# Kernel tuning notes

Measured on AMD Instinct MI355X. Metric: run time of the kernel, lower is better.

Reference implementation:

```python
import jax, jax.numpy as jnp
import numpy as np
from jax import lax

EPS = 1e-5
PH = PW = 2  # patch size

def _bn(x, g, b, m, v):
    # eval-mode BatchNorm2d on NCHW
    scale = (g / jnp.sqrt(v + EPS))[None, :, None, None]
    return (x - m[None, :, None, None]) * scale + b[None, :, None, None]

def _gn1(x, g, b):
    # GroupNorm(num_groups=1): normalize over (C,P,N) per sample
    mu = x.mean(axis=(1, 2, 3), keepdims=True)
    var = x.var(axis=(1, 2, 3), keepdims=True)
    return (x - mu) / jnp.sqrt(var + EPS) * g[None, :, None, None] + b[None, :, None, None]

def _conv1x1(x, w, b=None):
    y = jnp.einsum('oc,bcpn->bopn', w, x)
    if b is not None:
        y = y + b[None, :, None, None]
    return y

def _silu(x):
    return x * jax.nn.sigmoid(x)

def _lin_attn(x, qkv_w, qkv_b, out_w, out_b, D):
    # x: [B, D, P, N]
    qkv = _conv1x1(x, qkv_w, qkv_b)            # [B, 2D+1, P, N]
    q = qkv[:, :1]                              # [B, 1, P, N]
    k = qkv[:, 1:1 + D]                         # [B, D, P, N]
    v = qkv[:, 1 + D:]                          # [B, D, P, N]
    scores = jax.nn.softmax(q, axis=-1)         # softmax over patches N
    ctx = jnp.sum(k * scores, axis=-1, keepdims=True)  # [B, D, P, 1]
    out = jax.nn.relu(v) * ctx
    return _conv1x1(out, out_w, out_b)

def reference(x, dw_w, dw_bn_g, dw_bn_b, dw_bn_m, dw_bn_v, pw_w,
              gn1_g, gn1_b, qkv_w, qkv_b, out_w, out_b,
              gn2_g, gn2_b, ffn1_w, ffn1_b, ffn2_w, ffn2_b,
              gnf_g, gnf_b, proj_w, proj_bn_g, proj_bn_b, proj_bn_m, proj_bn_v):
    B, C, H, W = x.shape
    D = pw_w.shape[0]
    L = gn1_g.shape[0]
    # local representation: depthwise 3x3 conv + BN + SiLU, then 1x1 to attn dim
    y = lax.conv_general_dilated(x, dw_w, (1, 1), 'SAME',
                                 feature_group_count=C,
                                 dimension_numbers=('NCHW', 'OIHW', 'NCHW'))
    y = _silu(_bn(y, dw_bn_g, dw_bn_b, dw_bn_m, dw_bn_v))
    y = _conv1x1(y, pw_w)                       # [B, D, H, W]
    # unfold to [B, D, P, N] (non-overlapping patches, torch F.unfold ordering)
    nH, nW = H // PH, W // PW
    p = y.reshape(B, D, nH, PH, nW, PW).transpose(0, 1, 3, 5, 2, 4).reshape(B, D, PH * PW, nH * nW)
    # global representation: L pre-norm linear-attention + FFN blocks
    for i in range(L):
        p = p + _lin_attn(_gn1(p, gn1_g[i], gn1_b[i]), qkv_w[i], qkv_b[i], out_w[i], out_b[i], D)
        h = _gn1(p, gn2_g[i], gn2_b[i])
        h = _silu(_conv1x1(h, ffn1_w[i], ffn1_b[i]))
        h = _conv1x1(h, ffn2_w[i], ffn2_b[i])
        p = p + h
    p = _gn1(p, gnf_g, gnf_b)
    # fold back to [B, D, H, W]
    y = p.reshape(B, D, PH, PW, nH, nW).transpose(0, 1, 4, 2, 5, 3).reshape(B, D, H, W)
    # projection back to in_channels: 1x1 conv + BN (no act)
    y = _conv1x1(y, proj_w)
    y = _bn(y, proj_bn_g, proj_bn_b, proj_bn_m, proj_bn_v)
    return y

def setup_inputs() -> dict:
    key = jax.random.key(0)
    ks = iter(jax.random.split(key, 40))
    def rn(shape, s=0.05):
        return jax.random.normal(next(ks), shape, jnp.float32) * s
    B, C, H, W, D, F, L = 16, 256, 64, 64, 256, 512, 2
    return dict(
        x=jax.random.normal(next(ks), (B, C, H, W), jnp.float32),
        dw_w=rn((C, 1, 3, 3), 0.2),
        dw_bn_g=jnp.ones((C,), jnp.float32), dw_bn_b=jnp.zeros((C,), jnp.float32),
        dw_bn_m=rn((C,), 0.01), dw_bn_v=jnp.ones((C,), jnp.float32),
        pw_w=rn((D, C)),
        gn1_g=jnp.ones((L, D), jnp.float32), gn1_b=jnp.zeros((L, D), jnp.float32),
        qkv_w=rn((L, 2 * D + 1, D)), qkv_b=jnp.zeros((L, 2 * D + 1), jnp.float32),
        out_w=rn((L, D, D)), out_b=jnp.zeros((L, D), jnp.float32),
        gn2_g=jnp.ones((L, D), jnp.float32), gn2_b=jnp.zeros((L, D), jnp.float32),
        ffn1_w=rn((L, F, D)), ffn1_b=jnp.zeros((L, F), jnp.float32),
        ffn2_w=rn((L, D, F)), ffn2_b=jnp.zeros((L, D), jnp.float32),
        gnf_g=jnp.ones((D,), jnp.float32), gnf_b=jnp.zeros((D,), jnp.float32),
        proj_w=rn((C, D)),
        proj_bn_g=jnp.ones((C,), jnp.float32), proj_bn_b=jnp.zeros((C,), jnp.float32),
        proj_bn_m=rn((C,), 0.01), proj_bn_v=jnp.ones((C,), jnp.float32),
    )
```

## Files before the change

kernel.cpp:

```cpp
#include <hip/hip_runtime.h>
#include <hip/hip_bf16.h>
#include <stdint.h>


#define B_    16
#define C_    256
#define D_    256
#define NPIX  4096
#define NE_PB 1048576

typedef __attribute__((ext_vector_type(8))) short  short8;
typedef __attribute__((ext_vector_type(4))) short  short4v;
typedef __attribute__((ext_vector_type(4))) float  f32x4;
typedef __attribute__((ext_vector_type(2))) float  f32x2;

__device__ __forceinline__ float b2f(short s){
  return __uint_as_float(((unsigned)(unsigned short)s) << 16);
}
__device__ __forceinline__ short f2b(float f){
  __bf16 h = (__bf16)f;
  return *(short*)&h;
}
__device__ __forceinline__ float silu_f(float x){
  float e = __builtin_amdgcn_exp2f(-1.44269504f * x);
  return x * __builtin_amdgcn_rcpf(1.f + e);
}

__device__ __forceinline__ void gld16(const short* g, short* l){
  __builtin_amdgcn_global_load_lds(
      (const __attribute__((address_space(1))) void*)g,
      (__attribute__((address_space(3))) void*)l, 16, 0, 0);
}

__device__ __forceinline__ int pi2pix(int n){
  int p = n >> 10, idx = n & 1023;
  int h = ((idx >> 5) << 1) | (p >> 1);
  int w = ((idx & 31) << 1) | (p & 1);
  return h*64 + w;
}

__global__ void cvt6_k(const float* __restrict__ s0, const float* __restrict__ s1,
                       const float* __restrict__ s2, const float* __restrict__ s3,
                       const float* __restrict__ s4, const float* __restrict__ s5,
                       const float* __restrict__ g1, const float* __restrict__ g2,
                       const float* __restrict__ gf,
                       short* __restrict__ dst, float* __restrict__ stats){
  const int i = blockIdx.x*256 + threadIdx.x;
  if (blockIdx.x == 0 && threadIdx.x < 160) stats[threadIdx.x] = 0.f;
  if (i >= 1049088) return;
  float v;
  if      (i <  65536){ v = s0[i]; }
  else if (i < 328192){ int j = i -  65536;
                        v = s1[j] * g1[(j/131328)*256 + (j & 255)]; }
  else if (i < 459264){ v = s2[i - 328192]; }
  else if (i < 721408){ int j = i - 459264;
                        v = s3[j] * g2[(j >> 17)*256 + (j & 255)]; }
  else if (i < 983552){ v = s4[i - 721408]; }
  else               { int j = i - 983552;
                        v = s5[j] * gf[j & 255]; }
  dst[i] = f2b(v);
}

__global__ void fold_k(const float* __restrict__ qkvw, const float* __restrict__ f1w,
                       const float* __restrict__ pjw,
                       const float* __restrict__ g1, const float* __restrict__ b1,
                       const float* __restrict__ g2, const float* __restrict__ b2,
                       const float* __restrict__ gf, const float* __restrict__ bf,
                       float* __restrict__ uv){
  const int row = blockIdx.x;
  const int l = threadIdx.x;
  const float* W; const float* g; const float* bb;
  if (row < 1026){ int layer = row/513, o = row - layer*513;
    W = qkvw + (size_t)(layer*513 + o)*256; g = g1 + layer*256; bb = b1 + layer*256; }
  else if (row < 2050){ int r2 = row - 1026; int layer = r2 >> 9, o = r2 & 511;
    W = f1w + (size_t)(layer*512 + o)*256; g = g2 + layer*256; bb = b2 + layer*256; }
  else { int o = row - 2050; W = pjw + (size_t)o*256; g = gf; bb = bf; }
  float u = 0.f, v = 0.f;
#pragma unroll
  for (int k = 0; k < 4; ++k){
    const int c = l + k*64;
    const float w = W[c];
    u += w * g[c]; v += w * bb[c];
  }
#pragma unroll
  for (int o = 32; o > 0; o >>= 1){ u += __shfl_down(u, o); v += __shfl_down(v, o); }
  if (l == 0){ uv[row*2] = u; uv[row*2+1] = v; }
}

__global__ __launch_bounds__(256)
void dwconv_k(const float* __restrict__ X, const float* __restrict__ W,
              const float* __restrict__ G, const float* __restrict__ Bb,
              const float* __restrict__ Mn, const float* __restrict__ Vr,
              short* __restrict__ O){
  const int c = blockIdx.x, b = blockIdx.y;
  const int t = threadIdx.x;
  __shared__ float xs[66][68];
  if (t < 132){ int r = (t >= 66) ? 65 : 0; int cc = (t >= 66) ? t-66 : t; xs[r][cc] = 0.f; }
  if (t < 128){ int r = 1 + (t & 63); int cc = (t >> 6) ? 65 : 0; xs[r][cc] = 0.f; }
  const float* xp = X + ((size_t)(b*C_ + c)) * NPIX;
#pragma unroll
  for (int it = 0; it < 4; ++it){
    const int idx = it*256 + t;
    const int row = idx >> 4, cq = idx & 15;
    f32x4 v = *(const f32x4*)&xp[row*64 + cq*4];
    xs[row+1][cq*4+1] = v.x; xs[row+1][cq*4+2] = v.y;
    xs[row+1][cq*4+3] = v.z; xs[row+1][cq*4+4] = v.w;
  }
  float wgt[9];
#pragma unroll
  for (int j = 0; j < 9; ++j) wgt[j] = W[c*9 + j];
  const float scale = G[c] * rsqrtf(Vr[c] + 1e-5f);
  const float mu = Mn[c], bb = Bb[c];
  __syncthreads();
  const int tr = t >> 4, tc = t & 15;
  float win[6][6];
#pragma unroll
  for (int dr = 0; dr < 6; ++dr){
    f32x4 a = *(const f32x4*)&xs[tr*4+dr][tc*4];
    f32x2 bq = *(const f32x2*)&xs[tr*4+dr][tc*4+4];
    win[dr][0] = a.x; win[dr][1] = a.y; win[dr][2] = a.z; win[dr][3] = a.w;
    win[dr][4] = bq.x; win[dr][5] = bq.y;
  }
  short* op = O + ((size_t)(b*C_ + c)) * NPIX;
#pragma unroll
  for (int jr = 0; jr < 4; ++jr){
    short4v o;
#pragma unroll
    for (int jc = 0; jc < 4; ++jc){
      float s = 0.f;
#pragma unroll
      for (int dh = 0; dh < 3; ++dh)
#pragma unroll
        for (int dw = 0; dw < 3; ++dw)
          s += win[jr+dh][jc+dw] * wgt[dh*3+dw];
      float y = (s - mu) * scale + bb;
      o[jc] = f2b(silu_f(y));
    }
    *(short4v*)&op[(tr*4+jr)*64 + tc*4] = o;
  }
}

__global__ void transpose_k(const short* __restrict__ I, short* __restrict__ O){
  const int s0 = blockIdx.x*64, c0 = blockIdx.y*64, b = blockIdx.z;
  const int t = threadIdx.x;
  __shared__ short tile[64][68];
  const int hi = t >> 4, lo = t & 15;
#pragma unroll
  for (int cy = 0; cy < 4; ++cy){
    const int cl = cy*16 + hi;
    short4v v = *(const short4v*)&I[((size_t)(b*C_ + c0 + cl))*NPIX + s0 + lo*4];
    tile[lo*4+0][cl] = v.x; tile[lo*4+1][cl] = v.y;
    tile[lo*4+2][cl] = v.z; tile[lo*4+3][cl] = v.w;
  }
  __syncthreads();
#pragma unroll
  for (int py = 0; py < 4; ++py){
    const int pl = py*16 + hi;
    short4v v = *(const short4v*)&tile[pl][lo*4];
    *(short4v*)&O[((size_t)(b*NPIX + s0 + pl))*C_ + c0 + lo*4] = v;
  }
}

template<int EPI, int K, int FOLD, int GATHER>
__global__ __launch_bounds__(256, 3)
void gemm_k(const short* __restrict__ Wt, const short* __restrict__ X,
            const int M,
            const float* __restrict__ bias,
            short* __restrict__ P,
            short* __restrict__ Obf,
            float* __restrict__ Of32,
            const float* __restrict__ bng, const float* __restrict__ bnb,
            const float* __restrict__ bnm, const float* __restrict__ bnv,
            float* __restrict__ st,
            const float* __restrict__ uv, const float* __restrict__ stIn)
{
  constexpr int S = K / 64;
  const int nt = blockIdx.x;
  const int ct = blockIdx.y;
  const int b  = blockIdx.z;
  const int tid = threadIdx.x;
  const int ln = tid & 63, wv = tid >> 6;
  const int wx = wv & 1;
  const int wy = wv >> 1;
  const int lr = ln & 15, lq = ln >> 4;
  const int rl = ln >> 3, sp = ln & 7;
  const int sw = sp ^ rl;

  __shared__ __align__(16) char smem[33824];
  short* As = (short*)smem;
  short* Xs = (short*)(smem + 16384);
  float* CT = (float*)smem;
  float* red = (float*)(smem + 33792);

  const short* Wp = Wt + (size_t)(ct*128)*K;
  const short* Xp = X + ((size_t)b*NPIX + (size_t)nt*128) * K;

  const short* gw[4]; const short* gx[4]; short* lw[4]; short* lx[4];
#pragma unroll
  for (int j = 0; j < 4; ++j){
    const int row = 32*wv + 8*j + rl;
    gw[j] = Wp + (size_t)row*K + sw*8;
    if constexpr (GATHER)
      gx[j] = X + ((size_t)b*NPIX + pi2pix(nt*128 + row))*K + sw*8;
    else
      gx[j] = Xp + (size_t)row*K + sw*8;
    lw[j] = As + (4*wv + j)*512;
    lx[j] = Xs + (4*wv + j)*512;
  }

  f32x4 acc[4][4];
#pragma unroll
  for (int r = 0; r < 4; ++r)
#pragma unroll
    for (int c = 0; c < 4; ++c) acc[r][c] = (f32x4){0.f,0.f,0.f,0.f};

  for (int stp = 0; stp < S; ++stp){
    if (stp) __syncthreads();
#pragma unroll
    for (int j = 0; j < 4; ++j) gld16(gw[j] + stp*64, lw[j]);
#pragma unroll
    for (int j = 0; j < 4; ++j) gld16(gx[j] + stp*64, lx[j]);
    __syncthreads();
#pragma unroll
    for (int kk = 0; kk < 2; ++kk){
      const int seg = ((kk*4 + lq) ^ (lr & 7)) * 16;
      short8 aw[4], bx[4];
#pragma unroll
      for (int r = 0; r < 4; ++r)
        aw[r] = *(const short8*)((const char*)As + (wx*64 + r*16 + lr)*128 + seg);
#pragma unroll
      for (int c = 0; c < 4; ++c)
        bx[c] = *(const short8*)((const char*)Xs + (wy*64 + c*16 + lr)*128 + seg);
#pragma unroll
      for (int r = 0; r < 4; ++r)
#pragma unroll
        for (int c = 0; c < 4; ++c)
          acc[r][c] = __builtin_amdgcn_mfma_f32_16x16x32_bf16(aw[r], bx[c], acc[r][c], 0, 0, 0);
    }
  }

  const int ch8 = (tid & 15) * 8;
  float s_mul = 1.f;
  f32x4 be0 = (f32x4){0.f,0.f,0.f,0.f}, be1 = be0;
  if constexpr (EPI == 1 || EPI == 2 || EPI == 3 || EPI == 5){
    be0 = *(const f32x4*)&bias[ct*128 + ch8];
    be1 = *(const f32x4*)&bias[ct*128 + ch8 + 4];
  }
  if constexpr (FOLD && EPI != 4){
    const float mean = stIn[b*2]   * (1.f/NE_PB);
    const float m2   = stIn[b*2+1] * (1.f/NE_PB);
    const float inv  = rsqrtf(m2 - mean*mean + 1e-5f);
    s_mul = inv;
    const float muinv = mean * inv;
    const float* up = &uv[(size_t)(ct*128 + ch8)*2];
#pragma unroll
    for (int k = 0; k < 4; ++k){
      f32x2 p0 = *(const f32x2*)&up[k*2];
      f32x2 p1 = *(const f32x2*)&up[8 + k*2];
      be0[k] += p0.y - muinv*p0.x;
      be1[k] += p1.y - muinv*p1.x;
    }
  }

  float sm = 0.f, ss = 0.f;

  if constexpr (EPI != 4){
#pragma unroll
    for (int p = 0; p < 2; ++p){
      __syncthreads();
      if (wy == p){
#pragma unroll
        for (int r = 0; r < 4; ++r)
#pragma unroll
          for (int c = 0; c < 4; ++c)
            *(f32x4*)&CT[(c*16 + lr)*132 + wx*64 + r*16 + lq*4] = acc[r][c];
      }
      __syncthreads();
#pragma unroll
      for (int it = 0; it < 4; ++it){
        const int pixL = it*16 + (tid >> 4);
        f32x4 v0 = *(const f32x4*)&CT[pixL*132 + ch8];
        f32x4 v1 = *(const f32x4*)&CT[pixL*132 + ch8 + 4];
        if constexpr (EPI != 0){
          v0.x = v0.x*s_mul + be0.x; v0.y = v0.y*s_mul + be0.y;
          v0.z = v0.z*s_mul + be0.z; v0.w = v0.w*s_mul + be0.w;
          v1.x = v1.x*s_mul + be1.x; v1.y = v1.y*s_mul + be1.y;
          v1.z = v1.z*s_mul + be1.z; v1.w = v1.w*s_mul + be1.w;
        }
        int pixg = nt*128 + p*64 + pixL;
        if constexpr (EPI == 5) pixg = pi2pix(pixg);
        const size_t rowb = (size_t)b*NPIX + pixg;
        if constexpr (EPI == 0){
          short8 o;
          o[0]=f2b(v0.x); o[1]=f2b(v0.y); o[2]=f2b(v0.z); o[3]=f2b(v0.w);
          o[4]=f2b(v1.x); o[5]=f2b(v1.y); o[6]=f2b(v1.z); o[7]=f2b(v1.w);
          *(short8*)&P[rowb*256 + ct*128 + ch8] = o;
          sm += v0.x+v0.y+v0.z+v0.w + v1.x+v1.y+v1.z+v1.w;
          ss += v0.x*v0.x+v0.y*v0.y+v0.z*v0.z+v0.w*v0.w
              + v1.x*v1.x+v1.y*v1.y+v1.z*v1.z+v1.w*v1.w;
        } else if constexpr (EPI == 2 || EPI == 5){
          short* pp = &P[rowb*256 + ct*128 + ch8];
          short8 old = *(const short8*)pp;
          float n0 = b2f(old[0])+v0.x, n1 = b2f(old[1])+v0.y;
          float n2 = b2f(old[2])+v0.z, n3 = b2f(old[3])+v0.w;
          float n4 = b2f(old[4])+v1.x, n5 = b2f(old[5])+v1.y;
          float n6 = b2f(old[6])+v1.z, n7 = b2f(old[7])+v1.w;
          short8 o;
          o[0]=f2b(n0); o[1]=f2b(n1); o[2]=f2b(n2); o[3]=f2b(n3);
          o[4]=f2b(n4); o[5]=f2b(n5); o[6]=f2b(n6); o[7]=f2b(n7);
          *(short8*)pp = o;
          sm += n0+n1+n2+n3+n4+n5+n6+n7;
          ss += n0*n0+n1*n1+n2*n2+n3*n3+n4*n4+n5*n5+n6*n6+n7*n7;
        } else if constexpr (EPI == 1){
          short8 o;
          o[0]=f2b(v0.x); o[1]=f2b(v0.y); o[2]=f2b(v0.z); o[3]=f2b(v0.w);
          o[4]=f2b(v1.x); o[5]=f2b(v1.y); o[6]=f2b(v1.z); o[7]=f2b(v1.w);
          *(short8*)&Obf[rowb*(size_t)M + ct*128 + ch8] = o;
        } else {
          short8 o;
          o[0]=f2b(silu_f(v0.x)); o[1]=f2b(silu_f(v0.y));
          o[2]=f2b(silu_f(v0.z)); o[3]=f2b(silu_f(v0.w));
          o[4]=f2b(silu_f(v1.x)); o[5]=f2b(silu_f(v1.y));
          o[6]=f2b(silu_f(v1.z)); o[7]=f2b(silu_f(v1.w));
          *(short8*)&Obf[rowb*(size_t)M + ct*128 + ch8] = o;
        }
      }
    }
    if constexpr (EPI == 0 || EPI == 2 || EPI == 5){
#pragma unroll
      for (int o = 32; o > 0; o >>= 1){ sm += __shfl_down(sm, o); ss += __shfl_down(ss, o); }
      if (ln == 0){ red[wv*2] = sm; red[wv*2+1] = ss; }
      __syncthreads();
      if (tid == 0){
        atomicAdd(&st[b*2+0], red[0]+red[2]+red[4]+red[6]);
        atomicAdd(&st[b*2+1], red[1]+red[3]+red[5]+red[7]);
      }
    }
  } else {
    float muinv4 = 0.f;
    if constexpr (FOLD){
      const float mean = stIn[b*2]   * (1.f/NE_PB);
      const float m2   = stIn[b*2+1] * (1.f/NE_PB);
      const float inv  = rsqrtf(m2 - mean*mean + 1e-5f);
      s_mul = inv;
      muinv4 = mean * inv;
    }
#pragma unroll
    for (int p = 0; p < 2; ++p){
      __syncthreads();
      if (wx == p){
#pragma unroll
        for (int r = 0; r < 4; ++r)
#pragma unroll
          for (int c = 0; c < 4; ++c){
            const int pixL = wy*64 + c*16 + lr;
#pragma unroll
            for (int j = 0; j < 4; ++j)
              CT[(r*16 + lq*4 + j)*132 + pixL] = acc[r][c][j];
          }
      }
      __syncthreads();
#pragma unroll
      for (int it = 0; it < 8; ++it){
        const int idx = it*256 + tid;
        const int chL = idx >> 5, pq = (idx & 31)*4;
        const int chan = ct*128 + p*64 + chL;
        f32x4 v = *(const f32x4*)&CT[chL*132 + pq];
        const float sc = bng[chan] * rsqrtf(bnv[chan] + 1e-5f);
        const float mu = bnm[chan], bb = bnb[chan];
        float A = sc, Bc = -mu*sc + bb;
        if constexpr (FOLD){
          f32x2 uvp = *(const f32x2*)&uv[(size_t)chan*2];
          A = s_mul * sc;
          Bc = ((uvp.y - muinv4*uvp.x) - mu)*sc + bb;
        }
        f32x4 o;
        o.x = v.x*A + Bc; o.y = v.y*A + Bc;
        o.z = v.z*A + Bc; o.w = v.w*A + Bc;
        *(f32x4*)&Of32[((size_t)(b*C_ + chan))*NPIX + (size_t)nt*128 + pq] = o;
      }
    }
  }
}

__global__ void q_k(const short* __restrict__ P, const float* __restrict__ Wq,
                    const float* __restrict__ Gg, const float* __restrict__ Qb,
                    const float* __restrict__ uv, const float* __restrict__ stIn,
                    float* __restrict__ Q){
  const int lane = threadIdx.x & 63;
  const int pix = (blockIdx.x*256 + threadIdx.x) >> 6;
  const int b = pix >> 12, pi = pix & 4095;
  const int prow = pi2pix(pi);
  short4v u4 = *(const short4v*)&P[((size_t)b*NPIX + prow)*256 + lane*4];
  f32x4  w4 = *(const f32x4*)&Wq[lane*4];
  f32x4  g4 = *(const f32x4*)&Gg[lane*4];
  float s = b2f(u4.x)*w4.x*g4.x + b2f(u4.y)*w4.y*g4.y
          + b2f(u4.z)*w4.z*g4.z + b2f(u4.w)*w4.w*g4.w;
#pragma unroll
  for (int o = 32; o > 0; o >>= 1) s += __shfl_down(s, o);
  if (lane == 0){
    const float mean = stIn[b*2]   * (1.f/NE_PB);
    const float m2   = stIn[b*2+1] * (1.f/NE_PB);
    const float inv  = rsqrtf(m2 - mean*mean + 1e-5f);
    Q[pix] = inv*s + Qb[0] + uv[1] - inv*mean*uv[0];
  }
}

__global__ void softmax_k(const float* __restrict__ Q, float* __restrict__ S,
                          float* __restrict__ CT){
  const int bp = blockIdx.x;
  const int t = threadIdx.x;
  CT[bp*256 + t] = 0.f;
  float vals[4];
  float mx = -1e30f;
#pragma unroll
  for (int j = 0; j < 4; ++j){
    vals[j] = Q[bp*1024 + t + j*256];
    mx = fmaxf(mx, vals[j]);
  }
  __shared__ float red[4];
  const int lane = t & 63, wv = t >> 6;
#pragma unroll
  for (int o = 32; o > 0; o >>= 1) mx = fmaxf(mx, __shfl_down(mx, o));
  if (lane == 0) red[wv] = mx;
  __syncthreads();
  mx = fmaxf(fmaxf(red[0], red[1]), fmaxf(red[2], red[3]));
  __syncthreads();
  float sum = 0.f;
#pragma unroll
  for (int j = 0; j < 4; ++j){ vals[j] = expf(vals[j] - mx); sum += vals[j]; }
#pragma unroll
  for (int o = 32; o > 0; o >>= 1) sum += __shfl_down(sum, o);
  if (lane == 0) red[wv] = sum;
  __syncthreads();
  sum = red[0] + red[1] + red[2] + red[3];
  const float r = 1.f / sum;
#pragma unroll
  for (int j = 0; j < 4; ++j) S[bp*1024 + t + j*256] = vals[j]*r;
}

__global__ void ctx_k(const short* __restrict__ KV, const float* __restrict__ S,
                      float* __restrict__ CT){
  const int bp = blockIdx.x, ch = blockIdx.y;
  const int ln = threadIdx.x & 63, wv = threadIdx.x >> 6;
  const int j0 = ch*256 + wv*64;
  f32x4 acc = (f32x4){0.f,0.f,0.f,0.f};
  for (int jj = 0; jj < 64; jj += 4){
    f32x4 s4 = *(const f32x4*)&S[bp*1024 + j0 + jj];
#pragma unroll
    for (int u = 0; u < 4; ++u){
      short4v kv = *(const short4v*)&KV[((size_t)bp*1024 + j0 + jj + u)*512 + ln*4];
      const float s = s4[u];
      acc.x += b2f(kv.x)*s; acc.y += b2f(kv.y)*s;
      acc.z += b2f(kv.z)*s; acc.w += b2f(kv.w)*s;
    }
  }
  atomicAdd(&CT[bp*256 + ln*4 + 0], acc.x);
  atomicAdd(&CT[bp*256 + ln*4 + 1], acc.y);
  atomicAdd(&CT[bp*256 + ln*4 + 2], acc.z);
  atomicAdd(&CT[bp*256 + ln*4 + 3], acc.w);
}

__global__ void attn_in_k(const short* __restrict__ KV, const float* __restrict__ CT,
                          short* __restrict__ O){
  const size_t vid = (size_t)blockIdx.x*256 + threadIdx.x;
  const int c4 = (int)(vid & 63);
  const size_t r = vid >> 6;
  const int bp = (int)(r >> 10);
  short4v v4 = *(const short4v*)&KV[r*512 + 256 + c4*4];
  f32x4  cx = *(const f32x4*)&CT[bp*256 + c4*4];
  short4v o;
  o.x = f2b(fmaxf(b2f(v4.x), 0.f)*cx.x);
  o.y = f2b(fmaxf(b2f(v4.y), 0.f)*cx.y);
  o.z = f2b(fmaxf(b2f(v4.z), 0.f)*cx.z);
  o.w = f2b(fmaxf(b2f(v4.w), 0.f)*cx.w);
  *(short4v*)&O[r*256 + c4*4] = o;
}

extern "C" void kernel_launch(void* const* d_in, const int* in_sizes, int n_in,
                              void* d_out, int out_size, void* d_ws, size_t ws_size,
                              hipStream_t stream){
  const float* x      = (const float*)d_in[0];
  const float* dw_w   = (const float*)d_in[1];
  const float* dw_g   = (const float*)d_in[2];
  const float* dw_b   = (const float*)d_in[3];
  const float* dw_m   = (const float*)d_in[4];
  const float* dw_v   = (const float*)d_in[5];
  const float* pw_w   = (const float*)d_in[6];
  const float* gn1_g  = (const float*)d_in[7];
  const float* gn1_b  = (const float*)d_in[8];
  const float* qkv_w  = (const float*)d_in[9];
  const float* qkv_b  = (const float*)d_in[10];
  const float* out_w  = (const float*)d_in[11];
  const float* out_b  = (const float*)d_in[12];
  const float* gn2_g  = (const float*)d_in[13];
  const float* gn2_b  = (const float*)d_in[14];
  const float* ffn1_w = (const float*)d_in[15];
  const float* ffn1_b = (const float*)d_in[16];
  const float* ffn2_w = (const float*)d_in[17];
  const float* ffn2_b = (const float*)d_in[18];
  const float* gnf_g  = (const float*)d_in[19];
  const float* gnf_b  = (const float*)d_in[20];
  const float* proj_w = (const float*)d_in[21];
  const float* pbn_g  = (const float*)d_in[22];
  const float* pbn_b  = (const float*)d_in[23];
  const float* pbn_m  = (const float*)d_in[24];
  const float* pbn_v  = (const float*)d_in[25];
  float* out = (float*)d_out;

  uint8_t* w8 = (uint8_t*)d_ws;
  short* P     = (short*)(w8);
  short* bufA  = (short*)(w8 + 33554432);
  short* bufB  = (short*)(w8 + 67108864);
  short* wbase = (short*)(w8 + 134217728);
  short* w_pw  = wbase;
  short* w_qkv = wbase + 65536;
  short* w_out = wbase + 328192;
  short* w_f1  = wbase + 459264;
  short* w_f2  = wbase + 721408;
  short* w_pj  = wbase + 983552;
  float* qbuf  = (float*)(w8 + 136315904);
  float* scor  = (float*)(w8 + 136578048);
  float* ctxs  = (float*)(w8 + 136840192);
  float* stats = (float*)(w8 + 136905728);
  float* uvb   = (float*)(w8 + 136906368);

  cvt6_k<<<4098, 256, 0, stream>>>(pw_w, qkv_w, out_w, ffn1_w, ffn2_w, proj_w,
                                   gn1_g, gn2_g, gnf_g, wbase, stats);
  fold_k<<<2306, 64, 0, stream>>>(qkv_w, ffn1_w, proj_w,
                                  gn1_g, gn1_b, gn2_g, gn2_b, gnf_g, gnf_b, uvb);

  dwconv_k<<<dim3(256,16), 256, 0, stream>>>(x, dw_w, dw_g, dw_b, dw_m, dw_v, bufB);
  transpose_k<<<dim3(64,4,16), 256, 0, stream>>>(bufB, bufA);

  gemm_k<0,256,0,0><<<dim3(32,2,16), 256, 0, stream>>>(w_pw, bufA, 256, nullptr, P,
      nullptr, nullptr, nullptr, nullptr, nullptr, nullptr, stats + 0,
      nullptr, nullptr);

  for (int i = 0; i < 2; ++i){
    float* st1 = stats + (i == 0 ? 0 : 2)*32;
    q_k<<<16384, 256, 0, stream>>>(P, qkv_w + (size_t)i*513*256, gn1_g + i*256,
        qkv_b + i*513, uvb + (size_t)(i*513)*2, st1, qbuf);
    gemm_k<1,256,1,1><<<dim3(32,4,16), 256, 0, stream>>>(w_qkv + (i*513+1)*256, P, 512,
        qkv_b + i*513 + 1, nullptr, bufB, nullptr, nullptr, nullptr, nullptr, nullptr,
        nullptr, uvb + (size_t)(i*513+1)*2, st1);
    softmax_k<<<64, 256, 0, stream>>>(qbuf, scor, ctxs);
    ctx_k<<<dim3(64,4), 256, 0, stream>>>(bufB, scor, ctxs);
    attn_in_k<<<16384, 256, 0, stream>>>(bufB, ctxs, bufA);
    gemm_k<5,256,0,0><<<dim3(32,2,16), 256, 0, stream>>>(w_out + i*65536, bufA, 256,
        out_b + i*256, P, nullptr, nullptr, nullptr, nullptr, nullptr, nullptr,
        stats + (i == 0 ? 1 : 3)*32, nullptr, nullptr);
    float* st2 = stats + (i == 0 ? 1 : 3)*32;
    gemm_k<3,256,1,0><<<dim3(32,4,16), 256, 0, stream>>>(w_f1 + i*131072, P, 512,
        ffn1_b + i*512, nullptr, bufB, nullptr, nullptr, nullptr, nullptr, nullptr,
        nullptr, uvb + (size_t)(1026 + i*512)*2, st2);
    gemm_k<2,512,0,0><<<dim3(32,2,16), 256, 0, stream>>>(w_f2 + i*131072, bufB, 256,
        ffn2_b + i*256, P, nullptr, nullptr, nullptr, nullptr, nullptr, nullptr,
        stats + (i == 0 ? 2 : 4)*32, nullptr, nullptr);
  }

  gemm_k<4,256,1,0><<<dim3(32,2,16), 256, 0, stream>>>(w_pj, P, 256, nullptr,
      nullptr, nullptr, out, pbn_g, pbn_b, pbn_m, pbn_v, nullptr,
      uvb + (size_t)2050*2, stats + 4*32);

  (void)in_sizes; (void)n_in; (void)out_size; (void)ws_size;
}
```

Before: 581.9 us.

## Store residual stream in patch order and prefetch residual before GEMM main loop

New measurement: 580.0 us, median of 2. About the same (-0.3%).

```diff
diff --git a/kernel.cpp b/kernel.cpp
--- a/kernel.cpp
+++ b/kernel.cpp
@@ -37,6 +37,10 @@
   int h = ((idx >> 5) << 1) | (p >> 1);
   int w = ((idx & 31) << 1) | (p & 1);
   return h*64 + w;
+}
+__device__ __forceinline__ int pix2pi(int pix){
+  int h = pix >> 6, w = pix & 63;
+  return ((h & 1)*2 + (w & 1))*1024 + (h >> 1)*32 + (w >> 1);
 }
 
 __global__ void cvt6_k(const float* __restrict__ s0, const float* __restrict__ s1,
@@ -185,6 +189,7 @@
   const int lr = ln & 15, lq = ln >> 4;
   const int rl = ln >> 3, sp = ln & 7;
   const int sw = sp ^ rl;
+  const int ch8 = (tid & 15) * 8;
 
   __shared__ __align__(16) char smem[33824];
   short* As = (short*)smem;
@@ -200,14 +205,28 @@
   for (int j = 0; j < 4; ++j){
     const int row = 32*wv + 8*j + rl;
     gw[j] = Wp + (size_t)row*K + sw*8;
-    if constexpr (GATHER)
+    if constexpr (GATHER == 1)
       gx[j] = X + ((size_t)b*NPIX + pi2pix(nt*128 + row))*K + sw*8;
+    else if constexpr (GATHER == 2)
+      gx[j] = X + ((size_t)b*NPIX + pix2pi(nt*128 + row))*K + sw*8;
     else
       gx[j] = Xp + (size_t)row*K + sw*8;
     lw[j] = As + (4*wv + j)*512;
     lx[j] = Xs + (4*wv + j)*512;
   }
 
+  short8 oldv[2][4];
+  if constexpr (EPI == 2){
+#pragma unroll
+    for (int p = 0; p < 2; ++p)
+#pragma unroll
+      for (int it = 0; it < 4; ++it){
+        const int pixL = it*16 + (tid >> 4);
+        const size_t rowb = (size_t)b*NPIX + nt*128 + p*64 + pixL;
+        oldv[p][it] = *(const short8*)&P[rowb*256 + ct*128 + ch8];
+      }
+  }
+
   f32x4 acc[4][4];
 #pragma unroll
   for (int r = 0; r < 4; ++r)
@@ -239,12 +258,13 @@
     }
   }
 
-  const int ch8 = (tid & 15) * 8;
   float s_mul = 1.f;
   f32x4 be0 = (f32x4){0.f,0.f,0.f,0.f}, be1 = be0;
-  if constexpr (EPI == 1 || EPI == 2 || EPI == 3 || EPI == 5){
-    be0 = *(const f32x4*)&bias[ct*128 + ch8];
-    be1 = *(const f32x4*)&bias[ct*128 + ch8 + 4];
+  if constexpr (EPI == 1 || EPI == 2 || EPI == 3){
+    if constexpr (!FOLD){
+      be0 = *(const f32x4*)&bias[ct*128 + ch8];
+      be1 = *(const f32x4*)&bias[ct*128 + ch8 + 4];
+    }
   }
   if constexpr (FOLD && EPI != 4){
     const float mean = stIn[b*2]   * (1.f/NE_PB);
@@ -259,6 +279,14 @@
       f32x2 p1 = *(const f32x2*)&up[8 + k*2];
       be0[k] += p0.y - muinv*p0.x;
       be1[k] += p1.y - muinv*p1.x;
+    }
+    if constexpr (EPI == 1 || EPI == 2 || EPI == 3){
+      if (bias){
+        f32x4 bb0 = *(const f32x4*)&bias[ct*128 + ch8];
+        f32x4 bb1 = *(const f32x4*)&bias[ct*128 + ch8 + 4];
+        be0.x += bb0.x; be0.y += bb0.y; be0.z += bb0.z; be0.w += bb0.w;
+        be1.x += bb1.x; be1.y += bb1.y; be1.z += bb1.z; be1.w += bb1.w;
+      }
     }
   }
 
@@ -287,8 +315,7 @@
           v1.x = v1.x*s_mul + be1.x; v1.y = v1.y*s_mul + be1.y;
           v1.z = v1.z*s_mul + be1.z; v1.w = v1.w*s_mul + be1.w;
         }
-        int pixg = nt*128 + p*64 + pixL;
-        if constexpr (EPI == 5) pixg = pi2pix(pixg);
+        const int pixg = nt*128 + p*64 + pixL;
         const size_t rowb = (size_t)b*NPIX + pixg;
         if constexpr (EPI == 0){
           short8 o;
@@ -298,9 +325,8 @@
           sm += v0.x+v0.y+v0.z+v0.w + v1.x+v1.y+v1.z+v1.w;
           ss += v0.x*v0.x+v0.y*v0.y+v0.z*v0.z+v0.w*v0.w
               + v1.x*v1.x+v1.y*v1.y+v1.z*v1.z+v1.w*v1.w;
-        } else if constexpr (EPI == 2 || EPI == 5){
-          short* pp = &P[rowb*256 + ct*128 + ch8];
-          short8 old = *(const short8*)pp;
+        } else if constexpr (EPI == 2){
+          short8 old = oldv[p][it];
           float n0 = b2f(old[0])+v0.x, n1 = b2f(old[1])+v0.y;
           float n2 = b2f(old[2])+v0.z, n3 = b2f(old[3])+v0.w;
           float n4 = b2f(old[4])+v1.x, n5 = b2f(old[5])+v1.y;
@@ -308,7 +334,7 @@
           short8 o;
           o[0]=f2b(n0); o[1]=f2b(n1); o[2]=f2b(n2); o[3]=f2b(n3);
           o[4]=f2b(n4); o[5]=f2b(n5); o[6]=f2b(n6); o[7]=f2b(n7);
-          *(short8*)pp = o;
+          *(short8*)&P[rowb*256 + ct*128 + ch8] = o;
           sm += n0+n1+n2+n3+n4+n5+n6+n7;
           ss += n0*n0+n1*n1+n2*n2+n3*n3+n4*n4+n5*n5+n6*n6+n7*n7;
         } else if constexpr (EPI == 1){
@@ -326,7 +352,7 @@
         }
       }
     }
-    if constexpr (EPI == 0 || EPI == 2 || EPI == 5){
+    if constexpr (EPI == 0 || EPI == 2){
 #pragma unroll
       for (int o = 32; o > 0; o >>= 1){ sm += __shfl_down(sm, o); ss += __shfl_down(ss, o); }
       if (ln == 0){ red[wv*2] = sm; red[wv*2+1] = ss; }
@@ -389,9 +415,8 @@
                     float* __restrict__ Q){
   const int lane = threadIdx.x & 63;
   const int pix = (blockIdx.x*256 + threadIdx.x) >> 6;
-  const int b = pix >> 12, pi = pix & 4095;
-  const int prow = pi2pix(pi);
-  short4v u4 = *(const short4v*)&P[((size_t)b*NPIX + prow)*256 + lane*4];
+  const int b = pix >> 12;
+  short4v u4 = *(const short4v*)&P[(size_t)pix*256 + lane*4];
   f32x4  w4 = *(const f32x4*)&Wq[lane*4];
   f32x4  g4 = *(const f32x4*)&Gg[lane*4];
   float s = b2f(u4.x)*w4.x*g4.x + b2f(u4.y)*w4.y*g4.y
@@ -533,7 +558,7 @@
   dwconv_k<<<dim3(256,16), 256, 0, stream>>>(x, dw_w, dw_g, dw_b, dw_m, dw_v, bufB);
   transpose_k<<<dim3(64,4,16), 256, 0, stream>>>(bufB, bufA);
 
-  gemm_k<0,256,0,0><<<dim3(32,2,16), 256, 0, stream>>>(w_pw, bufA, 256, nullptr, P,
+  gemm_k<0,256,0,1><<<dim3(32,2,16), 256, 0, stream>>>(w_pw, bufA, 256, nullptr, P,
       nullptr, nullptr, nullptr, nullptr, nullptr, nullptr, stats + 0,
       nullptr, nullptr);
 
@@ -541,13 +566,13 @@
     float* st1 = stats + (i == 0 ? 0 : 2)*32;
     q_k<<<16384, 256, 0, stream>>>(P, qkv_w + (size_t)i*513*256, gn1_g + i*256,
         qkv_b + i*513, uvb + (size_t)(i*513)*2, st1, qbuf);
-    gemm_k<1,256,1,1><<<dim3(32,4,16), 256, 0, stream>>>(w_qkv + (i*513+1)*256, P, 512,
+    gemm_k<1,256,1,0><<<dim3(32,4,16), 256, 0, stream>>>(w_qkv + (i*513+1)*256, P, 512,
         qkv_b + i*513 + 1, nullptr, bufB, nullptr, nullptr, nullptr, nullptr, nullptr,
         nullptr, uvb + (size_t)(i*513+1)*2, st1);
     softmax_k<<<64, 256, 0, stream>>>(qbuf, scor, ctxs);
     ctx_k<<<dim3(64,4), 256, 0, stream>>>(bufB, scor, ctxs);
     attn_in_k<<<16384, 256, 0, stream>>>(bufB, ctxs, bufA);
-    gemm_k<5,256,0,0><<<dim3(32,2,16), 256, 0, stream>>>(w_out + i*65536, bufA, 256,
+    gemm_k<2,256,0,0><<<dim3(32,2,16), 256, 0, stream>>>(w_out + i*65536, bufA, 256,
         out_b + i*256, P, nullptr, nullptr, nullptr, nullptr, nullptr, nullptr,
         stats + (i == 0 ? 1 : 3)*32, nullptr, nullptr);
     float* st2 = stats + (i == 0 ? 1 : 3)*32;
@@ -559,7 +584,7 @@
         stats + (i == 0 ? 2 : 4)*32, nullptr, nullptr);
   }
 
-  gemm_k<4,256,1,0><<<dim3(32,2,16), 256, 0, stream>>>(w_pj, P, 256, nullptr,
+  gemm_k<4,256,1,2><<<dim3(32,2,16), 256, 0, stream>>>(w_pj, P, 256, nullptr,
       nullptr, nullptr, out, pbn_g, pbn_b, pbn_m, pbn_v, nullptr,
       uvb + (size_t)2050*2, stats + 4*32);
 
```
